# Kernel optimization log

Hardware: AMD Instinct MI355X
Metric: run time of the kernel (lower is better)

The kernel has to match this reference:

```python
import jax, jax.numpy as jnp
import numpy as np

N_NODES = 100000

def _graph_conv(x, src, dst, W, b, norm_src, norm_dst, activation):
    # DGL GraphConv, norm='both': D_out^{-1/2} on source, sum-aggregate, D_in^{-1/2} on dest
    h = x * norm_src[:, None]                       # [N, Din]
    # mult by W first when it reduces width (here Din >= Dout always) -> W then aggregate
    h = h @ W                                       # [N, Dout]
    m = jax.ops.segment_sum(h[src], dst, num_segments=N_NODES)  # gather + scatter-add
    out = m * norm_dst[:, None] + b
    if activation:
        out = jax.nn.relu(out)
    return out

def setup_inputs() -> dict:
    key = jax.random.key(0)
    ks = jax.random.split(key, 10)
    N, Din, H, Dout = N_NODES, 128, 128, 64
    E = 1600000
    x = jax.random.normal(ks[0], (N, Din), dtype=jnp.float32)
    src = jax.random.randint(ks[1], (E,), 0, N, dtype=jnp.int64)
    dst = jax.random.randint(ks[2], (E,), 0, N, dtype=jnp.int64)
    def glorot(k, fin, fout):
        s = jnp.sqrt(6.0 / (fin + fout)).astype(jnp.float32)
        return jax.random.uniform(k, (fin, fout), jnp.float32, -s, s)
    return {
        "x": x, "src": src, "dst": dst,
        "W1": glorot(ks[3], Din, H), "b1": jnp.zeros((H,), jnp.float32),
        "W2": glorot(ks[4], H, H),   "b2": jnp.zeros((H,), jnp.float32),
        "W3": glorot(ks[5], H, Dout),"b3": jnp.zeros((Dout,), jnp.float32),
    }

def reference(x, src, dst, W1, b1, W2, b2, W3, b3):
    ones = jnp.ones(src.shape[0], dtype=x.dtype)
    out_deg = jax.ops.segment_sum(ones, src, num_segments=N_NODES)
    in_deg = jax.ops.segment_sum(ones, dst, num_segments=N_NODES)
    norm_src = jax.lax.rsqrt(jnp.maximum(out_deg, 1.0))
    norm_dst = jax.lax.rsqrt(jnp.maximum(in_deg, 1.0))
    h = _graph_conv(x, src, dst, W1, b1, norm_src, norm_dst, True)
    h = _graph_conv(h, src, dst, W2, b2, norm_src, norm_dst, True)
    h = _graph_conv(h, src, dst, W3, b3, norm_src, norm_dst, False)
    return h
```

## Files before the change

kernel.cpp:

```cpp
#include <hip/hip_runtime.h>

#define NN 100000
#define NB 196
#define CH 4096

typedef short short8 __attribute__((ext_vector_type(8)));
typedef unsigned short u16x8 __attribute__((ext_vector_type(8)));
typedef float f32x4 __attribute__((ext_vector_type(4)));

__device__ inline unsigned short f2bf(float x) {
    unsigned u = __float_as_uint(x);
    unsigned r = (u + 0x7FFF + ((u >> 16) & 1)) >> 16;
    return (unsigned short)r;
}
__device__ inline float bf2f(unsigned short h) {
    return __uint_as_float(((unsigned)h) << 16);
}

__global__ __launch_bounds__(256) void k_bhist2(const int* __restrict__ src,
    const int* __restrict__ dst, int* __restrict__ bcntS, int* __restrict__ bcntD, int E)
{
    __shared__ int hs[NB], hd[NB];
    int t = threadIdx.x;
    if (t < NB) { hs[t] = 0; hd[t] = 0; }
    __syncthreads();
    int stride = gridDim.x * 256;
    for (int e = blockIdx.x * 256 + t; e < E; e += stride) {
        atomicAdd(&hs[src[e] >> 9], 1);
        atomicAdd(&hd[dst[e] >> 9], 1);
    }
    __syncthreads();
    if (t < NB) {
        if (hs[t]) atomicAdd(&bcntS[t], hs[t]);
        if (hd[t]) atomicAdd(&bcntD[t], hd[t]);
    }
}

__global__ __launch_bounds__(256) void k_bscan2(const int* __restrict__ bcntS,
    const int* __restrict__ bcntD, int* __restrict__ bbaseS, int* __restrict__ gcurS,
    int* __restrict__ bbaseD, int* __restrict__ gcurD)
{
    __shared__ int s[256];
    int t = threadIdx.x;
    int cD = (t < NB) ? bcntD[t] : 0;
    int cS = (t < NB) ? bcntS[t] : 0;

    int v = cD;
    s[t] = v;
    __syncthreads();
#pragma unroll
    for (int off = 1; off < 256; off <<= 1) {
        int x = (t >= off) ? s[t - off] : 0;
        __syncthreads(); s[t] += x; __syncthreads();
    }
    if (t < NB) { int e = s[t] - v; bbaseD[t] = e; gcurD[t] = e; }
    __syncthreads();

    v = cS;
    s[t] = v;
    __syncthreads();
#pragma unroll
    for (int off = 1; off < 256; off <<= 1) {
        int x = (t >= off) ? s[t - off] : 0;
        __syncthreads(); s[t] += x; __syncthreads();
    }
    if (t < NB) { int e = s[t] - v; bbaseS[t] = e; gcurS[t] = e; }
}

__global__ __launch_bounds__(256) void k_bscatter3(const int* __restrict__ src,
    const int* __restrict__ dst, int* __restrict__ gcurD, int* __restrict__ gcurS,
    unsigned* __restrict__ tmpD, unsigned* __restrict__ tmpS, int E)
{
    __shared__ int cntD[NB], cntS[NB];
    __shared__ int runD[NB], runS[NB];
    int t = threadIdx.x;
    if (t < NB) { cntD[t] = 0; cntS[t] = 0; }
    __syncthreads();

    const int e0 = blockIdx.x * CH;
    int sv[16], dv[16];
    int offD[16], offS[16];
#pragma unroll
    for (int i = 0; i < 16; i++) {
        int e = e0 + i * 256 + t;
        if (e < E) { sv[i] = src[e]; dv[i] = dst[e]; }
    }
#pragma unroll
    for (int i = 0; i < 16; i++) {
        int e = e0 + i * 256 + t;
        if (e < E) {
            offD[i] = atomicAdd(&cntD[dv[i] >> 9], 1);
            offS[i] = atomicAdd(&cntS[sv[i] >> 9], 1);
        }
    }
    __syncthreads();
    if (t < NB) {
        int c = cntD[t];
        if (c) runD[t] = atomicAdd(&gcurD[t], c);
        c = cntS[t];
        if (c) runS[t] = atomicAdd(&gcurS[t], c);
    }
    __syncthreads();
#pragma unroll
    for (int i = 0; i < 16; i++) {
        int e = e0 + i * 256 + t;
        if (e < E) {
            int bD = dv[i] >> 9;
            tmpD[runD[bD] + offD[i]] = (unsigned)sv[i] | ((unsigned)(dv[i] & 511) << 17);
            int bS = sv[i] >> 9;
            tmpS[runS[bS] + offS[i]] = (unsigned)(sv[i] & 511);
        }
    }
}

__global__ __launch_bounds__(256) void k_cntS(const int* __restrict__ bbaseS,
    const int* __restrict__ bcntS, const unsigned* __restrict__ tmpS,
    float* __restrict__ ns, int N)
{
    __shared__ int cnt[512];
    int b = blockIdx.x, t = threadIdx.x;
    cnt[t] = 0; cnt[t + 256] = 0;
    __syncthreads();
    int beg = bbaseS[b], end = beg + bcntS[b];
    for (int e = beg + t; e < end; e += 256)
        atomicAdd(&cnt[tmpS[e]], 1);
    __syncthreads();
    int nb = b << 9;
    for (int i = t; i < 512; i += 256) {
        int n = nb + i;
        if (n < N) ns[n] = rsqrtf(fmaxf((float)cnt[i], 1.0f));
    }
}

__global__ __launch_bounds__(256) void k_csrD(const int* __restrict__ bbaseD,
    const int* __restrict__ bcntD, const unsigned* __restrict__ tmpD,
    int* __restrict__ degI, float* __restrict__ nd,
    int* __restrict__ rowptr, int* __restrict__ srcIdx, int N)
{
    __shared__ int cnt[8192];
    __shared__ int sblk[256];
    int b = blockIdx.x, t = threadIdx.x;
    for (int i = t; i < 8192; i += 256) cnt[i] = 0;
    __syncthreads();
    int beg = bbaseD[b], end = beg + bcntD[b];
    for (int e = beg + t; e < end; e += 256) {
        unsigned v = tmpD[e];
        int dl = v >> 17;
        int s  = (int)(v & 0x1FFFFu);
        atomicAdd(&cnt[(dl << 4) | (s >> 13)], 1);
    }
    __syncthreads();
    int loc[32];
    int sum = 0;
#pragma unroll
    for (int i = 0; i < 32; i++) { loc[i] = sum; sum += cnt[t * 32 + i]; }
    sblk[t] = sum;
    __syncthreads();
#pragma unroll
    for (int off = 1; off < 256; off <<= 1) {
        int x = (t >= off) ? sblk[t - off] : 0;
        __syncthreads(); sblk[t] += x; __syncthreads();
    }
    int base = beg + sblk[t] - sum;
    int v0 = loc[16];
    int v1 = sum - loc[16];
    int nb = b << 9;
    int n0 = nb + 2 * t, n1 = n0 + 1;
    if (n0 < N) { rowptr[n0] = base;           degI[n0] = v0; nd[n0] = rsqrtf(fmaxf((float)v0, 1.f)); }
    if (n1 < N) { rowptr[n1] = base + loc[16]; degI[n1] = v1; nd[n1] = rsqrtf(fmaxf((float)v1, 1.f)); }
#pragma unroll
    for (int i = 0; i < 32; i++) cnt[t * 32 + i] = base + loc[i];
    __syncthreads();
    for (int e = beg + t; e < end; e += 256) {
        unsigned v = tmpD[e];
        int dl = v >> 17;
        int s  = (int)(v & 0x1FFFFu);
        int pos = atomicAdd(&cnt[(dl << 4) | (s >> 13)], 1);
        srcIdx[pos] = s;
    }
}

template<int DOUT>
__global__ __launch_bounds__(256) void k_prepW(const float* __restrict__ W,
    unsigned short* __restrict__ Wh, unsigned short* __restrict__ Wl)
{
    int idx = blockIdx.x * 256 + threadIdx.x;
    if (idx >= 128 * DOUT) return;
    int c = idx % DOUT;
    int k = idx / DOUT;
    float w = W[idx];
    unsigned short hi = f2bf(w);
    unsigned short lo = f2bf(w - bf2f(hi));
    int boff = c * 256 + ((2 * k) ^ ((c & 7) << 4));
    *(unsigned short*)((char*)Wh + boff) = hi;
    *(unsigned short*)((char*)Wl + boff) = lo;
}

template<int DOUT>
__global__ __launch_bounds__(256) void k_gemm_mfma(
    const float* __restrict__ in,
    const unsigned short* __restrict__ Wth, const unsigned short* __restrict__ Wtl,
    const float* __restrict__ ns,
    unsigned short* __restrict__ out, int N)
{
    constexpr int NT = DOUT / 16;
    __shared__ __align__(16) unsigned short Wh[DOUT * 128];
    __shared__ __align__(16) unsigned short Wl[DOUT * 128];

    const int t = threadIdx.x;
    const int w = t >> 6, l = t & 63;

#pragma unroll
    for (int i = 0; i < DOUT * 256 / 4096; i++) {
        int off = i * 4096 + t * 16;
        *(float4*)((char*)Wh + off) = *(const float4*)((const char*)Wth + off);
        *(float4*)((char*)Wl + off) = *(const float4*)((const char*)Wtl + off);
    }

    const int rl   = l & 15;
    const int kgrp = l >> 4;
    const int row  = blockIdx.x * 64 + w * 16 + rl;
    const int rowc = row < N ? row : N - 1;
    const float* arow = in + (size_t)rowc * 128;

    float av[4][8];
#pragma unroll
    for (int ks = 0; ks < 4; ks++) {
        int kb = ks * 32 + kgrp * 8;
        float4 v0 = *(const float4*)(arow + kb);
        float4 v1 = *(const float4*)(arow + kb + 4);
        av[ks][0] = v0.x; av[ks][1] = v0.y; av[ks][2] = v0.z; av[ks][3] = v0.w;
        av[ks][4] = v1.x; av[ks][5] = v1.y; av[ks][6] = v1.z; av[ks][7] = v1.w;
    }
    float nsv = ns[rowc];
    short8 Ah[4], Al[4];
#pragma unroll
    for (int ks = 0; ks < 4; ks++)
#pragma unroll
        for (int j = 0; j < 8; j++) {
            float v = av[ks][j] * nsv;
            unsigned short hi = f2bf(v);
            Ah[ks][j] = (short)hi;
            Al[ks][j] = (short)f2bf(v - bf2f(hi));
        }

    __syncthreads();

    f32x4 acc[NT];
#pragma unroll
    for (int tt = 0; tt < NT; tt++) acc[tt] = (f32x4){0.f, 0.f, 0.f, 0.f};

#pragma unroll
    for (int ks = 0; ks < 4; ks++) {
        int kbyte = ks * 64 + kgrp * 16;
#pragma unroll
        for (int tt = 0; tt < NT; tt++) {
            int c = tt * 16 + rl;
            int boff = c * 256 + (kbyte ^ ((c & 7) << 4));
            short8 Bh = *(short8*)((char*)Wh + boff);
            short8 Bl = *(short8*)((char*)Wl + boff);
            acc[tt] = __builtin_amdgcn_mfma_f32_16x16x32_bf16(Ah[ks], Bh, acc[tt], 0, 0, 0);
            acc[tt] = __builtin_amdgcn_mfma_f32_16x16x32_bf16(Al[ks], Bh, acc[tt], 0, 0, 0);
            acc[tt] = __builtin_amdgcn_mfma_f32_16x16x32_bf16(Ah[ks], Bl, acc[tt], 0, 0, 0);
        }
    }

    const int orow = blockIdx.x * 64 + w * 16 + kgrp * 4;
#pragma unroll
    for (int r = 0; r < 4; r++) {
        if (orow + r < N) {
#pragma unroll
            for (int tt = 0; tt < NT; tt++)
                out[(size_t)(orow + r) * DOUT + tt * 16 + rl] = f2bf(acc[tt][r]);
        }
    }
}

__global__ __launch_bounds__(256) void k_agg_epi(
    const int* __restrict__ rowptr, const int* __restrict__ cnt,
    const int* __restrict__ srcIdx, const unsigned short* __restrict__ h,
    const float* __restrict__ nd, const float* __restrict__ ns,
    const float* __restrict__ bias,
    unsigned short* __restrict__ out, int N)
{
    int t = threadIdx.x;
    int node = blockIdx.x * 16 + (t >> 4);
    if (node >= N) return;
    int c = (t & 15) * 8;

    int beg = rowptr[node];
    int end = beg + cnt[node];
    float acc[8] = {0.f, 0.f, 0.f, 0.f, 0.f, 0.f, 0.f, 0.f};
    int e = beg;
    for (; e + 1 < end; e += 2) {
        int s0 = srcIdx[e], s1 = srcIdx[e + 1];
        u16x8 v0 = *(const u16x8*)&h[(size_t)s0 * 128 + c];
        u16x8 v1 = *(const u16x8*)&h[(size_t)s1 * 128 + c];
#pragma unroll
        for (int j = 0; j < 8; j++) acc[j] += bf2f(v0[j]) + bf2f(v1[j]);
    }
    if (e < end) {
        int s0 = srcIdx[e];
        u16x8 v0 = *(const u16x8*)&h[(size_t)s0 * 128 + c];
#pragma unroll
        for (int j = 0; j < 8; j++) acc[j] += bf2f(v0[j]);
    }
    float ndv = nd[node], nsv = ns[node];
    float4 b0 = *(const float4*)(bias + c);
    float4 b1 = *(const float4*)(bias + c + 4);
    float bb[8] = {b0.x, b0.y, b0.z, b0.w, b1.x, b1.y, b1.z, b1.w};
    u16x8 o;
#pragma unroll
    for (int j = 0; j < 8; j++)
        o[j] = f2bf(fmaxf(acc[j] * ndv + bb[j], 0.f) * nsv);
    *(u16x8*)&out[(size_t)node * 128 + c] = o;
}

template<int DOUT>
__global__ __launch_bounds__(256) void k_gemm_bf(
    const unsigned short* __restrict__ in,
    const unsigned short* __restrict__ Wth, const unsigned short* __restrict__ Wtl,
    unsigned short* __restrict__ out, int N)
{
    constexpr int NT = DOUT / 16;
    __shared__ __align__(16) unsigned short Wh[DOUT * 128];
    __shared__ __align__(16) unsigned short Wl[DOUT * 128];

    const int t = threadIdx.x;
    const int w = t >> 6, l = t & 63;

#pragma unroll
    for (int i = 0; i < DOUT * 256 / 4096; i++) {
        int off = i * 4096 + t * 16;
        *(float4*)((char*)Wh + off) = *(const float4*)((const char*)Wth + off);
        *(float4*)((char*)Wl + off) = *(const float4*)((const char*)Wtl + off);
    }

    const int rl   = l & 15;
    const int kgrp = l >> 4;
    const int row  = blockIdx.x * 64 + w * 16 + rl;
    const int rowc = row < N ? row : N - 1;
    const unsigned short* arow = in + (size_t)rowc * 128;

    short8 Ah[4];
#pragma unroll
    for (int ks = 0; ks < 4; ks++)
        Ah[ks] = *(const short8*)(arow + ks * 32 + kgrp * 8);

    __syncthreads();

    f32x4 acc[NT];
#pragma unroll
    for (int tt = 0; tt < NT; tt++) acc[tt] = (f32x4){0.f, 0.f, 0.f, 0.f};

#pragma unroll
    for (int ks = 0; ks < 4; ks++) {
        int kbyte = ks * 64 + kgrp * 16;
#pragma unroll
        for (int tt = 0; tt < NT; tt++) {
            int c = tt * 16 + rl;
            int boff = c * 256 + (kbyte ^ ((c & 7) << 4));
            short8 Bh = *(short8*)((char*)Wh + boff);
            short8 Bl = *(short8*)((char*)Wl + boff);
            acc[tt] = __builtin_amdgcn_mfma_f32_16x16x32_bf16(Ah[ks], Bh, acc[tt], 0, 0, 0);
            acc[tt] = __builtin_amdgcn_mfma_f32_16x16x32_bf16(Ah[ks], Bl, acc[tt], 0, 0, 0);
        }
    }

    const int orow = blockIdx.x * 64 + w * 16 + kgrp * 4;
#pragma unroll
    for (int r = 0; r < 4; r++) {
        if (orow + r < N) {
#pragma unroll
            for (int tt = 0; tt < NT; tt++)
                out[(size_t)(orow + r) * DOUT + tt * 16 + rl] = f2bf(acc[tt][r]);
        }
    }
}

template<int D>
__global__ __launch_bounds__(256) void k_agg_final(
    const int* __restrict__ rowptr, const int* __restrict__ cnt,
    const int* __restrict__ srcIdx, const unsigned short* __restrict__ h,
    const float* __restrict__ nd, const float* __restrict__ b3,
    float* __restrict__ m, int N)
{
    constexpr int TPN = D / 8;
    constexpr int NPB = 256 / TPN;
    int t = threadIdx.x;
    int node = blockIdx.x * NPB + t / TPN;
    if (node >= N) return;
    int c = (t % TPN) * 8;

    int beg = rowptr[node];
    int end = beg + cnt[node];
    float acc[8] = {0.f, 0.f, 0.f, 0.f, 0.f, 0.f, 0.f, 0.f};
    int e = beg;
    for (; e + 1 < end; e += 2) {
        int s0 = srcIdx[e], s1 = srcIdx[e + 1];
        u16x8 v0 = *(const u16x8*)&h[(size_t)s0 * D + c];
        u16x8 v1 = *(const u16x8*)&h[(size_t)s1 * D + c];
#pragma unroll
        for (int j = 0; j < 8; j++) acc[j] += bf2f(v0[j]) + bf2f(v1[j]);
    }
    if (e < end) {
        int s0 = srcIdx[e];
        u16x8 v0 = *(const u16x8*)&h[(size_t)s0 * D + c];
#pragma unroll
        for (int j = 0; j < 8; j++) acc[j] += bf2f(v0[j]);
    }
    float ndv = nd[node];
#pragma unroll
    for (int j = 0; j < 8; j++) acc[j] = acc[j] * ndv + b3[c + j];
    float4* mp = (float4*)&m[(size_t)node * D + c];
    mp[0] = make_float4(acc[0], acc[1], acc[2], acc[3]);
    mp[1] = make_float4(acc[4], acc[5], acc[6], acc[7]);
}

extern "C" void kernel_launch(void* const* d_in, const int* in_sizes, int n_in,
                              void* d_out, int out_size, void* d_ws, size_t ws_size,
                              hipStream_t stream) {
    const float* x  = (const float*)d_in[0];
    const int*   src = (const int*)d_in[1];
    const int*   dst = (const int*)d_in[2];
    const float* W1 = (const float*)d_in[3];
    const float* b1 = (const float*)d_in[4];
    const float* W2 = (const float*)d_in[5];
    const float* b2 = (const float*)d_in[6];
    const float* W3 = (const float*)d_in[7];
    const float* b3 = (const float*)d_in[8];
    float* out = (float*)d_out;

    const int N = NN;
    const int E = in_sizes[1];

    char* ws = (char*)d_ws;
    unsigned short* bufA = (unsigned short*)ws;
    unsigned short* bufB = (unsigned short*)(ws + (size_t)N * 128 * 4);
    unsigned* tmpD = (unsigned*)bufA;
    unsigned* tmpS = (unsigned*)bufB;
    char*  p     = ws + (size_t)N * 128 * 4 * 2;
    float* ns    = (float*)p;              p += (size_t)N * 4;
    float* nd    = (float*)p;              p += (size_t)N * 4;
    int*   degI  = (int*)p;                p += (size_t)N * 4;
    int*   rowp  = (int*)p;                p += (size_t)N * 4;
    int*   srcIdx= (int*)p;                p += (size_t)E * 4;
    unsigned short* W1h = (unsigned short*)p; p += 128 * 128 * 2;
    unsigned short* W1l = (unsigned short*)p; p += 128 * 128 * 2;
    unsigned short* W2h = (unsigned short*)p; p += 128 * 128 * 2;
    unsigned short* W2l = (unsigned short*)p; p += 128 * 128 * 2;
    unsigned short* W3h = (unsigned short*)p; p += 64 * 128 * 2;
    unsigned short* W3l = (unsigned short*)p; p += 64 * 128 * 2;
    int* bcntS = (int*)p;                  p += 256 * 4;
    int* bcntD = (int*)p;                  p += 256 * 4;
    int* bbaseS= (int*)p;                  p += 256 * 4;
    int* bbaseD= (int*)p;                  p += 256 * 4;
    int* gcurS = (int*)p;                  p += 256 * 4;
    int* gcurD = (int*)p;                  p += 256 * 4;
    unsigned short* bufC = (unsigned short*)p;

    k_prepW<128><<<64, 256, 0, stream>>>(W1, W1h, W1l);
    k_prepW<128><<<64, 256, 0, stream>>>(W2, W2h, W2l);
    k_prepW<64><<<32, 256, 0, stream>>>(W3, W3h, W3l);

    hipMemsetAsync(bcntS, 0, 2 * 256 * 4, stream);
    k_bhist2<<<192, 256, 0, stream>>>(src, dst, bcntS, bcntD, E);
    k_bscan2<<<1, 256, 0, stream>>>(bcntS, bcntD, bbaseS, gcurS, bbaseD, gcurD);
    k_bscatter3<<<(E + CH - 1) / CH, 256, 0, stream>>>(src, dst, gcurD, gcurS, tmpD, tmpS, E);
    k_cntS<<<NB, 256, 0, stream>>>(bbaseS, bcntS, tmpS, ns, N);
    k_csrD<<<NB, 256, 0, stream>>>(bbaseD, bcntD, tmpD, degI, nd, rowp, srcIdx, N);

    const int gemm_grid = (N + 63) / 64;
    const int agg16     = (N + 15) / 16;
    const int agg64     = (N + 31) / 32;

    k_gemm_mfma<128><<<gemm_grid, 256, 0, stream>>>(x, W1h, W1l, ns, bufA, N);

    k_agg_epi<<<agg16, 256, 0, stream>>>(rowp, degI, srcIdx, bufA, nd, ns, b1, bufB, N);
    k_gemm_bf<128><<<gemm_grid, 256, 0, stream>>>(bufB, W2h, W2l, bufC, N);

    k_agg_epi<<<agg16, 256, 0, stream>>>(rowp, degI, srcIdx, bufC, nd, ns, b2, bufB, N);
    k_gemm_bf<64><<<gemm_grid, 256, 0, stream>>>(bufB, W3h, W3l, bufA, N);

    k_agg_final<64><<<agg64, 256, 0, stream>>>(rowp, degI, srcIdx, bufA, nd, b3, out, N);
}
```

Baseline: 307.8 us.

## Merge preprocessing launches, drop memset via partial histograms, unroll gathers by four

The three weight-prep kernels become one launch. The global-atomic histogram plus memset is replaced by per-block partial histograms that the single-block scan kernel sums. The source-degree and CSR-build kernels are merged into one grid so they run concurrently. The aggregation loops are unrolled to four gathers per iteration for more memory-level parallelism, at the cost of a serial 192-iteration reduction in the scan block and more registers.

```diff
diff --git a/kernel.cpp b/kernel.cpp
--- a/kernel.cpp
+++ b/kernel.cpp
@@ -3,6 +3,7 @@
 #define NN 100000
 #define NB 196
 #define CH 4096
+#define HB 192
 
 typedef short short8 __attribute__((ext_vector_type(8)));
 typedef unsigned short u16x8 __attribute__((ext_vector_type(8)));
@@ -17,33 +18,37 @@
     return __uint_as_float(((unsigned)h) << 16);
 }
 
-__global__ __launch_bounds__(256) void k_bhist2(const int* __restrict__ src,
-    const int* __restrict__ dst, int* __restrict__ bcntS, int* __restrict__ bcntD, int E)
+__global__ __launch_bounds__(256) void k_bhist2p(const int* __restrict__ src,
+    const int* __restrict__ dst, int* __restrict__ partS, int* __restrict__ partD, int E)
 {
     __shared__ int hs[NB], hd[NB];
     int t = threadIdx.x;
     if (t < NB) { hs[t] = 0; hd[t] = 0; }
     __syncthreads();
-    int stride = gridDim.x * 256;
+    int stride = HB * 256;
     for (int e = blockIdx.x * 256 + t; e < E; e += stride) {
         atomicAdd(&hs[src[e] >> 9], 1);
         atomicAdd(&hd[dst[e] >> 9], 1);
     }
     __syncthreads();
-    if (t < NB) {
-        if (hs[t]) atomicAdd(&bcntS[t], hs[t]);
-        if (hd[t]) atomicAdd(&bcntD[t], hd[t]);
-    }
-}
-
-__global__ __launch_bounds__(256) void k_bscan2(const int* __restrict__ bcntS,
-    const int* __restrict__ bcntD, int* __restrict__ bbaseS, int* __restrict__ gcurS,
+    partS[blockIdx.x * 256 + t] = (t < NB) ? hs[t] : 0;
+    partD[blockIdx.x * 256 + t] = (t < NB) ? hd[t] : 0;
+}
+
+__global__ __launch_bounds__(256) void k_bscan2(const int* __restrict__ partS,
+    const int* __restrict__ partD,
+    int* __restrict__ bcntS, int* __restrict__ bcntD,
+    int* __restrict__ bbaseS, int* __restrict__ gcurS,
     int* __restrict__ bbaseD, int* __restrict__ gcurD)
 {
     __shared__ int s[256];
     int t = threadIdx.x;
-    int cD = (t < NB) ? bcntD[t] : 0;
-    int cS = (t < NB) ? bcntS[t] : 0;
+    int cS = 0, cD = 0;
+    for (int i = 0; i < HB; i++) {
+        cS += partS[i * 256 + t];
+        cD += partD[i * 256 + t];
+    }
+    if (t < NB) { bcntS[t] = cS; bcntD[t] = cD; }
 
     int v = cD;
     s[t] = v;
@@ -113,33 +118,33 @@
     }
 }
 
-__global__ __launch_bounds__(256) void k_cntS(const int* __restrict__ bbaseS,
-    const int* __restrict__ bcntS, const unsigned* __restrict__ tmpS,
-    float* __restrict__ ns, int N)
-{
-    __shared__ int cnt[512];
-    int b = blockIdx.x, t = threadIdx.x;
-    cnt[t] = 0; cnt[t + 256] = 0;
-    __syncthreads();
-    int beg = bbaseS[b], end = beg + bcntS[b];
-    for (int e = beg + t; e < end; e += 256)
-        atomicAdd(&cnt[tmpS[e]], 1);
-    __syncthreads();
-    int nb = b << 9;
-    for (int i = t; i < 512; i += 256) {
-        int n = nb + i;
-        if (n < N) ns[n] = rsqrtf(fmaxf((float)cnt[i], 1.0f));
-    }
-}
-
-__global__ __launch_bounds__(256) void k_csrD(const int* __restrict__ bbaseD,
-    const int* __restrict__ bcntD, const unsigned* __restrict__ tmpD,
-    int* __restrict__ degI, float* __restrict__ nd,
+__global__ __launch_bounds__(256) void k_build(
+    const int* __restrict__ bbaseD, const int* __restrict__ bcntD, const unsigned* __restrict__ tmpD,
+    const int* __restrict__ bbaseS, const int* __restrict__ bcntS, const unsigned* __restrict__ tmpS,
+    int* __restrict__ degI, float* __restrict__ nd, float* __restrict__ ns,
     int* __restrict__ rowptr, int* __restrict__ srcIdx, int N)
 {
     __shared__ int cnt[8192];
     __shared__ int sblk[256];
-    int b = blockIdx.x, t = threadIdx.x;
+    int t = threadIdx.x;
+
+    if (blockIdx.x >= NB) {
+        int b = blockIdx.x - NB;
+        cnt[t] = 0; cnt[t + 256] = 0;
+        __syncthreads();
+        int beg = bbaseS[b], end = beg + bcntS[b];
+        for (int e = beg + t; e < end; e += 256)
+            atomicAdd(&cnt[tmpS[e]], 1);
+        __syncthreads();
+        int nb = b << 9;
+        for (int i = t; i < 512; i += 256) {
+            int n = nb + i;
+            if (n < N) ns[n] = rsqrtf(fmaxf((float)cnt[i], 1.0f));
+        }
+        return;
+    }
+
+    int b = blockIdx.x;
     for (int i = t; i < 8192; i += 256) cnt[i] = 0;
     __syncthreads();
     int beg = bbaseD[b], end = beg + bcntD[b];
@@ -180,11 +185,17 @@
     }
 }
 
-template<int DOUT>
-__global__ __launch_bounds__(256) void k_prepW(const float* __restrict__ W,
-    unsigned short* __restrict__ Wh, unsigned short* __restrict__ Wl)
-{
-    int idx = blockIdx.x * 256 + threadIdx.x;
+__global__ __launch_bounds__(256) void k_prepW_all(
+    const float* __restrict__ W1, const float* __restrict__ W2, const float* __restrict__ W3,
+    unsigned short* __restrict__ W1h, unsigned short* __restrict__ W1l,
+    unsigned short* __restrict__ W2h, unsigned short* __restrict__ W2l,
+    unsigned short* __restrict__ W3h, unsigned short* __restrict__ W3l)
+{
+    int b = blockIdx.x;
+    const float* W; unsigned short *Wh, *Wl; int DOUT, idx;
+    if (b < 64)       { W = W1; Wh = W1h; Wl = W1l; DOUT = 128; idx = b * 256 + threadIdx.x; }
+    else if (b < 128) { W = W2; Wh = W2h; Wl = W2l; DOUT = 128; idx = (b - 64) * 256 + threadIdx.x; }
+    else              { W = W3; Wh = W3h; Wl = W3l; DOUT = 64;  idx = (b - 128) * 256 + threadIdx.x; }
     if (idx >= 128 * DOUT) return;
     int c = idx % DOUT;
     int k = idx / DOUT;
@@ -292,14 +303,17 @@
     int end = beg + cnt[node];
     float acc[8] = {0.f, 0.f, 0.f, 0.f, 0.f, 0.f, 0.f, 0.f};
     int e = beg;
-    for (; e + 1 < end; e += 2) {
-        int s0 = srcIdx[e], s1 = srcIdx[e + 1];
+    for (; e + 3 < end; e += 4) {
+        int s0 = srcIdx[e], s1 = srcIdx[e + 1], s2 = srcIdx[e + 2], s3 = srcIdx[e + 3];
         u16x8 v0 = *(const u16x8*)&h[(size_t)s0 * 128 + c];
         u16x8 v1 = *(const u16x8*)&h[(size_t)s1 * 128 + c];
-#pragma unroll
-        for (int j = 0; j < 8; j++) acc[j] += bf2f(v0[j]) + bf2f(v1[j]);
-    }
-    if (e < end) {
+        u16x8 v2 = *(const u16x8*)&h[(size_t)s2 * 128 + c];
+        u16x8 v3 = *(const u16x8*)&h[(size_t)s3 * 128 + c];
+#pragma unroll
+        for (int j = 0; j < 8; j++)
+            acc[j] += (bf2f(v0[j]) + bf2f(v1[j])) + (bf2f(v2[j]) + bf2f(v3[j]));
+    }
+    for (; e < end; e++) {
         int s0 = srcIdx[e];
         u16x8 v0 = *(const u16x8*)&h[(size_t)s0 * 128 + c];
 #pragma unroll
@@ -396,14 +410,17 @@
     int end = beg + cnt[node];
     float acc[8] = {0.f, 0.f, 0.f, 0.f, 0.f, 0.f, 0.f, 0.f};
     int e = beg;
-    for (; e + 1 < end; e += 2) {
-        int s0 = srcIdx[e], s1 = srcIdx[e + 1];
+    for (; e + 3 < end; e += 4) {
+        int s0 = srcIdx[e], s1 = srcIdx[e + 1], s2 = srcIdx[e + 2], s3 = srcIdx[e + 3];
         u16x8 v0 = *(const u16x8*)&h[(size_t)s0 * D + c];
         u16x8 v1 = *(const u16x8*)&h[(size_t)s1 * D + c];
-#pragma unroll
-        for (int j = 0; j < 8; j++) acc[j] += bf2f(v0[j]) + bf2f(v1[j]);
-    }
-    if (e < end) {
+        u16x8 v2 = *(const u16x8*)&h[(size_t)s2 * D + c];
+        u16x8 v3 = *(const u16x8*)&h[(size_t)s3 * D + c];
+#pragma unroll
+        for (int j = 0; j < 8; j++)
+            acc[j] += (bf2f(v0[j]) + bf2f(v1[j])) + (bf2f(v2[j]) + bf2f(v3[j]));
+    }
+    for (; e < end; e++) {
         int s0 = srcIdx[e];
         u16x8 v0 = *(const u16x8*)&h[(size_t)s0 * D + c];
 #pragma unroll
@@ -457,18 +474,17 @@
     int* bbaseD= (int*)p;                  p += 256 * 4;
     int* gcurS = (int*)p;                  p += 256 * 4;
     int* gcurD = (int*)p;                  p += 256 * 4;
+    int* partS = (int*)p;                  p += (size_t)HB * 256 * 4;
+    int* partD = (int*)p;                  p += (size_t)HB * 256 * 4;
     unsigned short* bufC = (unsigned short*)p;
 
-    k_prepW<128><<<64, 256, 0, stream>>>(W1, W1h, W1l);
-    k_prepW<128><<<64, 256, 0, stream>>>(W2, W2h, W2l);
-    k_prepW<64><<<32, 256, 0, stream>>>(W3, W3h, W3l);
-
-    hipMemsetAsync(bcntS, 0, 2 * 256 * 4, stream);
-    k_bhist2<<<192, 256, 0, stream>>>(src, dst, bcntS, bcntD, E);
-    k_bscan2<<<1, 256, 0, stream>>>(bcntS, bcntD, bbaseS, gcurS, bbaseD, gcurD);
+    k_prepW_all<<<160, 256, 0, stream>>>(W1, W2, W3, W1h, W1l, W2h, W2l, W3h, W3l);
+
+    k_bhist2p<<<HB, 256, 0, stream>>>(src, dst, partS, partD, E);
+    k_bscan2<<<1, 256, 0, stream>>>(partS, partD, bcntS, bcntD, bbaseS, gcurS, bbaseD, gcurD);
     k_bscatter3<<<(E + CH - 1) / CH, 256, 0, stream>>>(src, dst, gcurD, gcurS, tmpD, tmpS, E);
-    k_cntS<<<NB, 256, 0, stream>>>(bbaseS, bcntS, tmpS, ns, N);
-    k_csrD<<<NB, 256, 0, stream>>>(bbaseD, bcntD, tmpD, degI, nd, rowp, srcIdx, N);
+    k_build<<<2 * NB, 256, 0, stream>>>(bbaseD, bcntD, tmpD, bbaseS, bcntS, tmpS,
+                                        degI, nd, ns, rowp, srcIdx, N);
 
     const int gemm_grid = (N + 63) / 64;
     const int agg16     = (N + 15) / 16;
```

Measured after the change: 284.6 us. -7.5%, faster.
